# Performance work log

Hardware: AMD Instinct MI355X
Metric: run time of the kernel (lower is better)

## Reference

```python
import jax, jax.numpy as jnp
import numpy as np


def rel_to_abs(x):
    """[b, hh, L, 2L-1] -> [b, hh, L, L] via pad/reshape trick."""
    b, hh, L, _ = x.shape
    x = jnp.pad(x, ((0, 0), (0, 0), (0, 0), (0, 1)))          # [b,hh,L,2L]
    flat = x.reshape(b, hh, L * 2 * L)
    flat = jnp.pad(flat, ((0, 0), (0, 0), (0, L - 1)))
    final = flat.reshape(b, hh, L + 1, 2 * L - 1)
    return final[:, :, :L, L - 1:]                             # [b,hh,L,L]


def relative_logits_1d(q, rel_k, transpose_mask):
    # q: [b, n, x, y, d]; rel_k: [2y-1, d]
    b, n, x, y, d = q.shape
    rel = jnp.einsum('bnxyd,md->bnxym', q, rel_k)
    rel = rel.reshape(b, n * x, y, 2 * y - 1)
    rel = rel_to_abs(rel)                                      # [b, n*x, y, y]
    rel = rel.reshape(b, n, x, y, y)
    rel = jnp.broadcast_to(rel[:, :, :, None, :, :], (b, n, x, x, y, y))
    return jnp.transpose(rel, transpose_mask)


def relative_logits(q, rel_emb_w, rel_emb_h):
    logits_w = relative_logits_1d(q, rel_emb_w, (0, 1, 2, 4, 3, 5))
    q_t = jnp.transpose(q, (0, 1, 3, 2, 4))  # swap h/w
    logits_h = relative_logits_1d(q_t, rel_emb_h, (0, 1, 4, 2, 5, 3))
    return logits_h + logits_w  # [b,n,h,w,h,w]


def setup_inputs() -> dict:
    key = jax.random.key(0)
    k1, k2, k3, k4, k5 = jax.random.split(key, 5)
    B, N, H, W, D = 4, 4, 48, 48, 32
    std = D ** (-0.5)
    return {
        'q': jax.random.normal(k1, (B, N, H, W, D), jnp.float32),
        'k': jax.random.normal(k2, (B, N, H, W, D), jnp.float32),
        'v': jax.random.normal(k3, (B, N, H, W, D), jnp.float32),
        'rel_emb_w': jax.random.normal(k4, (2 * W - 1, D), jnp.float32) * std,
        'rel_emb_h': jax.random.normal(k5, (2 * H - 1, D), jnp.float32) * std,
    }


def reference(q, k, v, rel_emb_w, rel_emb_h):
    bs, heads, h, w, dim = q.shape
    q = q * dim ** (-0.5)
    logits = jnp.einsum('bnhwd,bnpqd->bnhwpq', q, k)
    logits = logits + relative_logits(q, rel_emb_w, rel_emb_h)
    weights = jax.nn.softmax(logits.reshape(bs, heads, h, w, h * w), axis=-1)
    weights = weights.reshape(bs, heads, h, w, h, w)
    attn_out = jnp.einsum('bnhwpq,bnpqd->bhwnd', weights, v)
    # fold_heads=True
    return attn_out.reshape(bs, h, w, heads * dim)
```

## Files before the change

### kernel.cpp

```cpp
#include <hip/hip_runtime.h>
#include <hip/hip_bf16.h>


typedef __attribute__((ext_vector_type(8))) short bf16x8;
typedef __attribute__((ext_vector_type(4))) float f32x4;

#define DEVFN __device__ __forceinline__

#if __has_builtin(__builtin_amdgcn_exp2f)
#define EXP2(x) __builtin_amdgcn_exp2f(x)
#else
#define EXP2(x) exp2f(x)
#endif

constexpr int H_ = 48, W_ = 48, D_ = 32;
constexpr int L_ = H_ * W_;
constexpr int BN_ = 16;

constexpr int QB2 = 48;
constexpr int QT2 = L_ / QB2;
constexpr int NWG2 = BN_ * QT2;

constexpr size_t WE_Q = 0;
constexpr size_t WE_K = 1179648;
constexpr size_t WE_V = 2359296;
constexpr size_t WE_R = 3538944;
constexpr size_t WS_NEED = (WE_R + 2 * 6 * 64 * 8) * 2;

DEVFN unsigned short f2bf(float f) {
  unsigned u = __float_as_uint(f);
  return (unsigned short)((u + 0x7fffu + ((u >> 16) & 1u)) >> 16);
}
DEVFN unsigned pk2(float lo, float hi) {
  return (unsigned)f2bf(lo) | ((unsigned)f2bf(hi) << 16);
}
DEVFN unsigned pkcvt(float lo, float hi) {
  __hip_bfloat162 h = __float22bfloat162_rn(make_float2(lo, hi));
  union { __hip_bfloat162 h2; unsigned u; } cv; cv.h2 = h;
  return cv.u;
}

template <int CTRL>
DEVFN float dppf(float x) {
  return __int_as_float(__builtin_amdgcn_update_dpp(0, __float_as_int(x), CTRL, 0xF, 0xF, true));
}
DEVFN float rowmax16(float x) {
  x = fmaxf(x, dppf<0x128>(x));
  x = fmaxf(x, dppf<0x124>(x));
  x = fmaxf(x, dppf<0x122>(x));
  x = fmaxf(x, dppf<0x121>(x));
  return x;
}
DEVFN float rowsum16(float x) {
  x += dppf<0x128>(x);
  x += dppf<0x124>(x);
  x += dppf<0x122>(x);
  x += dppf<0x121>(x);
  return x;
}

__global__ __launch_bounds__(256)
void prep_kernel(const float* __restrict__ Q, const float* __restrict__ K,
                 const float* __restrict__ V, const float* __restrict__ RW,
                 const float* __restrict__ RH, unsigned short* __restrict__ ws)
{
  __shared__ __align__(16) float Vl[3072];
  const int bid = blockIdx.x, tid = threadIdx.x;
  const float QS = 0.17677669529663687f * 1.4426950408889634f;
  if (bid < 576) {
    size_t e = ((size_t)bid * 256 + tid) * 8;
    const float* s = Q + e;
    float4 a = *(const float4*)s, c = *(const float4*)(s + 4);
    uint4 wv;
    wv.x = pkcvt(a.x * QS, a.y * QS); wv.y = pkcvt(a.z * QS, a.w * QS);
    wv.z = pkcvt(c.x * QS, c.y * QS); wv.w = pkcvt(c.z * QS, c.w * QS);
    *(uint4*)(ws + WE_Q + e) = wv;
  } else if (bid < 1152) {
    int idx = (bid - 576) * 256 + tid;
    int lane = idx & 63, t = idx >> 6;
    int l15 = lane & 15, lg = lane >> 4;
    int bn = t / 144, t16 = t % 144;
    int it = t16 / 6, kb = t16 % 6;
    int kbp = kb >> 1, f = kb & 1;
    int key96 = kbp * 32 + (l15 >> 2) * 8 + f * 4 + (l15 & 3);
    const float* s = K + ((size_t)(bn * L_ + it * 96 + key96) * D_ + lg * 8);
    float4 a = *(const float4*)s, c = *(const float4*)(s + 4);
    uint4 wv;
    wv.x = pkcvt(a.x, a.y); wv.y = pkcvt(a.z, a.w);
    wv.z = pkcvt(c.x, c.y); wv.w = pkcvt(c.z, c.w);
    *(uint4*)(ws + WE_K + (size_t)idx * 8) = wv;
  } else if (bid < 1536) {
    const int tile = bid - 1152;
    const float* src = V + (size_t)tile * 96 * D_;
    #pragma unroll
    for (int u = 0; u < 3; ++u)
      ((float4*)Vl)[tid + u * 256] = ((const float4*)src)[tid + u * 256];
    __syncthreads();
    unsigned short* dst = ws + WE_V + (size_t)tile * 3072;
    #pragma unroll
    for (int u = 0; u < 2; ++u) {
      const int f2i = tid + u * 256;
      if (f2i < 384) {
        const int f2 = f2i >> 6, lane = f2i & 63;
        const int l15 = lane & 15, lg = lane >> 4;
        const int kbp = f2 >> 1, half = f2 & 1;
        const int d = half * 16 + l15;
        float fv[8];
        #pragma unroll
        for (int j = 0; j < 8; ++j)
          fv[j] = Vl[(kbp * 32 + lg * 8 + j) * 32 + d];
        uint4 wv;
        wv.x = pkcvt(fv[0], fv[1]); wv.y = pkcvt(fv[2], fv[3]);
        wv.z = pkcvt(fv[4], fv[5]); wv.w = pkcvt(fv[6], fv[7]);
        *(uint4*)(dst + (size_t)f2i * 8) = wv;
      }
    }
  } else {
    int t = (bid - 1536) * 256 + tid;
    if (t < 768) {
      int tbl = t / 384, rem = t % 384, jb = rem / 64, lane = rem % 64;
      int l15 = lane & 15, lg = lane >> 4;
      int j = jb * 16 + l15;
      int jc = (j > 94) ? 94 : j;
      const float* s = (tbl ? RW : RH) + jc * D_ + lg * 8;
      float4 a = *(const float4*)s, c = *(const float4*)(s + 4);
      uint4 wv;
      wv.x = pkcvt(a.x, a.y); wv.y = pkcvt(a.z, a.w);
      wv.z = pkcvt(c.x, c.y); wv.w = pkcvt(c.z, c.w);
      *(uint4*)(ws + WE_R + (size_t)t * 8) = wv;
    }
  }
}

__global__ __launch_bounds__(192, 4)
void relattn9(const unsigned short* __restrict__ ws, float* __restrict__ OUT)
{
  __shared__ __align__(16) float BhT[48 * 50];
  __shared__ __align__(16) float BwT[48 * 52];
  __shared__ __align__(16) float Pp[3 * 2 * 3 * 256];
  __shared__ __align__(16) float Ppl[3 * 3 * 64];

  const unsigned short* Qb = ws + WE_Q;
  const unsigned short* Kf = ws + WE_K;
  const unsigned short* Vf = ws + WE_V;
  const unsigned short* Rf = ws + WE_R;

  const int bid = blockIdx.x;
  const int wg  = (bid & 7) * (NWG2 / 8) + (bid >> 3);
  const int bn  = wg / QT2;
  const int qb  = (wg % QT2) * QB2;
  const int b   = bn >> 2, n = bn & 3;

  const int tid  = threadIdx.x;
  const int w    = tid >> 6;
  const int lane = tid & 63;
  const int l15  = lane & 15;
  const int lg   = lane >> 4;

  const f32x4 z4 = {0.f, 0.f, 0.f, 0.f};

  bf16x8 qfr[3];
  #pragma unroll
  for (int qf = 0; qf < 3; ++qf)
    qfr[qf] = *(const bf16x8*)(Qb + (size_t)(bn * L_ + qb + qf * 16 + l15) * D_ + lg * 8);

  #pragma unroll
  for (int jb = 0; jb < 6; ++jb) {
    bf16x8 rhf = *(const bf16x8*)(Rf + ((0 * 6 + jb) * 64 + lane) * 8);
    bf16x8 rwf = *(const bf16x8*)(Rf + ((1 * 6 + jb) * 64 + lane) * 8);
    f32x4 mh = __builtin_amdgcn_mfma_f32_16x16x32_bf16(qfr[w], rhf, z4, 0, 0, 0);
    f32x4 mw = __builtin_amdgcn_mfma_f32_16x16x32_bf16(qfr[w], rwf, z4, 0, 0, 0);
    const int j = jb * 16 + l15;
    if (j < 95) {
      #pragma unroll
      for (int r = 0; r < 4; ++r) {
        const int qg = qb + w * 16 + lg * 4 + r;
        const int row = w * 16 + lg * 4 + r;
        const int p  = j - 47 + qg / 48;
        if (p >= 0 && p < 48)  BhT[row * 50 + p]  = mh[r];
        const int ww = j - 47 + qg % 48;
        if (ww >= 0 && ww < 48) BwT[row * 52 + ww] = mw[r];
      }
    }
  }
  __syncthreads();

  int baset = w * 32 + lg * 8; if (baset >= 48) baset -= 48;
  const float* bwq0 = &BwT[(0 * 16 + l15) * 52 + baset];
  const float* bwq1 = &BwT[(1 * 16 + l15) * 52 + baset];
  const float* bwq2 = &BwT[(2 * 16 + l15) * 52 + baset];
  const float* bhq0 = &BhT[(0 * 16 + l15) * 50];
  const float* bhq1 = &BhT[(1 * 16 + l15) * 50];
  const float* bhq2 = &BhT[(2 * 16 + l15) * 50];
  const bool keylo = (w == 0) | ((w == 1) & (lg < 2));

  const unsigned short* KfW = Kf + (size_t)bn * 24 * 3072 + (size_t)(2 * w) * 512 + (size_t)lane * 8;
  const unsigned short* VfW = Vf + (size_t)bn * 24 * 3072 + (size_t)(2 * w) * 512 + (size_t)lane * 8;

  f32x4 acc[2][3] = {{z4, z4, z4}, {z4, z4, z4}};
  float l_acc[3] = {0.f, 0.f, 0.f};

  bf16x8 kfA[2], vfA[2], kfB[2], vfB[2];

#define LOADIT(kfX, vfX, itv) do {                                          \
    const unsigned short* kt_ = KfW + (size_t)(itv) * 3072;                 \
    const unsigned short* vt_ = VfW + (size_t)(itv) * 3072;                 \
    kfX[0] = *(const bf16x8*)(kt_);                                         \
    kfX[1] = *(const bf16x8*)(kt_ + 512);                                   \
    vfX[0] = *(const bf16x8*)(vt_);                                         \
    vfX[1] = *(const bf16x8*)(vt_ + 512);                                   \
  } while (0)

#define COMPUTE(itv, kfX, vfX) do {                                         \
    _Pragma("unroll") for (int qf = 0; qf < 3; ++qf) {                      \
      const float* bhq_ = (qf == 0) ? bhq0 : ((qf == 1) ? bhq1 : bhq2);     \
      const float* bwq_ = (qf == 0) ? bwq0 : ((qf == 1) ? bwq1 : bwq2);     \
      const float2 bh2_ = *(const float2*)(bhq_ + (itv) * 2);               \
      const float bf_ = EXP2(keylo ? bh2_.x : bh2_.y);                      \
      f32x4 cin0 = *(const f32x4*)(bwq_);                                   \
      f32x4 cin1 = *(const f32x4*)(bwq_ + 4);                               \
      f32x4 s0 = __builtin_amdgcn_mfma_f32_16x16x32_bf16(kfX[0], qfr[qf], cin0, 0, 0, 0); \
      f32x4 s1 = __builtin_amdgcn_mfma_f32_16x16x32_bf16(kfX[1], qfr[qf], cin1, 0, 0, 0); \
      const float e0 = EXP2(s0[0]) * bf_, e1 = EXP2(s0[1]) * bf_;           \
      const float e2 = EXP2(s0[2]) * bf_, e3 = EXP2(s0[3]) * bf_;           \
      const float e4 = EXP2(s1[0]) * bf_, e5 = EXP2(s1[1]) * bf_;           \
      const float e6 = EXP2(s1[2]) * bf_, e7 = EXP2(s1[3]) * bf_;           \
      l_acc[qf] += (((e0 + e1) + (e2 + e3)) + ((e4 + e5) + (e6 + e7)));     \
      union { unsigned u[4]; bf16x8 v; } pf_;                               \
      pf_.u[0] = pkcvt(e0, e1); pf_.u[1] = pkcvt(e2, e3);                   \
      pf_.u[2] = pkcvt(e4, e5); pf_.u[3] = pkcvt(e6, e7);                   \
      acc[0][qf] = __builtin_amdgcn_mfma_f32_16x16x32_bf16(vfX[0], pf_.v, acc[0][qf], 0, 0, 0); \
      acc[1][qf] = __builtin_amdgcn_mfma_f32_16x16x32_bf16(vfX[1], pf_.v, acc[1][qf], 0, 0, 0); \
    }                                                                       \
  } while (0)

  LOADIT(kfA, vfA, 0);
  for (int it2 = 0; it2 < 12; ++it2) {
    const int itA = it2 * 2;
    __builtin_amdgcn_sched_barrier(0);
    LOADIT(kfB, vfB, itA + 1);
    __builtin_amdgcn_sched_barrier(0);
    COMPUTE(itA, kfA, vfA);
    __builtin_amdgcn_sched_barrier(0);
    LOADIT(kfA, vfA, itA + 2);
    __builtin_amdgcn_sched_barrier(0);
    COMPUTE(itA + 1, kfB, vfB);
  }
#undef LOADIT
#undef COMPUTE

  #pragma unroll
  for (int dh = 0; dh < 2; ++dh)
    #pragma unroll
    for (int qf = 0; qf < 3; ++qf)
      *(f32x4*)&Pp[((w * 2 + dh) * 3 + qf) * 256 + lane * 4] = acc[dh][qf];
  #pragma unroll
  for (int qf = 0; qf < 3; ++qf)
    Ppl[(w * 3 + qf) * 64 + lane] = l_acc[qf];
  __syncthreads();

  f32x4 o0 = *(const f32x4*)&Pp[((0 * 2 + 0) * 3 + w) * 256 + lane * 4];
  f32x4 o1 = *(const f32x4*)&Pp[((0 * 2 + 1) * 3 + w) * 256 + lane * 4];
  #pragma unroll
  for (int wp = 1; wp < 3; ++wp) {
    o0 += *(const f32x4*)&Pp[((wp * 2 + 0) * 3 + w) * 256 + lane * 4];
    o1 += *(const f32x4*)&Pp[((wp * 2 + 1) * 3 + w) * 256 + lane * 4];
  }
  float ls = Ppl[(0 * 3 + w) * 64 + lane] + Ppl[(1 * 3 + w) * 64 + lane]
           + Ppl[(2 * 3 + w) * 64 + lane];
  ls += __shfl_xor(ls, 16);
  ls += __shfl_xor(ls, 32);
  const float inv = __builtin_amdgcn_rcpf(ls);
  const int ql = qb + w * 16 + l15;
  const int hql = ql / 48, wql = ql % 48;
  float* op = OUT + ((size_t)(b * 48 + hql) * 48 + wql) * 128 + n * 32 + lg * 4;
  *(float4*)op        = make_float4(o0[0] * inv, o0[1] * inv, o0[2] * inv, o0[3] * inv);
  *(float4*)(op + 16) = make_float4(o1[0] * inv, o1[1] * inv, o1[2] * inv, o1[3] * inv);
}

__global__ __launch_bounds__(256, 2)
void relattn_kernel(const float* __restrict__ Q, const float* __restrict__ K,
                    const float* __restrict__ V, const float* __restrict__ RW,
                    const float* __restrict__ RH, float* __restrict__ OUT)
{
  __shared__ __align__(16) unsigned short Klds[64][40];
  __shared__ __align__(16) unsigned       VT[32][36];
  __shared__ __align__(16) unsigned short Plds[4][16][72];
  __shared__ __align__(16) float          Bh[64][49];
  __shared__ __align__(16) float          Bw[64][49];

  const int bid = blockIdx.x;
  const int wg  = (bid & 7) * 72 + (bid >> 3);
  const int bn  = wg / 36;
  const int qb  = (wg % 36) * 64;
  const int b   = bn >> 2, n = bn & 3;

  const int tid  = threadIdx.x;
  const int wave = tid >> 6;
  const int lane = tid & 63;
  const int l15  = lane & 15;
  const int lg   = lane >> 4;

  const float QS = 0.17677669529663687f * 1.4426950408889634f;
  const int qi = qb + wave * 16 + l15;
  bf16x8 qfrag;
  {
    const float* qr = Q + ((bn * L_ + qi) * D_ + lg * 8);
    float4 a = *(const float4*)qr;
    float4 c = *(const float4*)(qr + 4);
    qfrag[0] = (short)f2bf(a.x * QS); qfrag[1] = (short)f2bf(a.y * QS);
    qfrag[2] = (short)f2bf(a.z * QS); qfrag[3] = (short)f2bf(a.w * QS);
    qfrag[4] = (short)f2bf(c.x * QS); qfrag[5] = (short)f2bf(c.y * QS);
    qfrag[6] = (short)f2bf(c.z * QS); qfrag[7] = (short)f2bf(c.w * QS);
  }
  const f32x4 z4 = {0.f, 0.f, 0.f, 0.f};
  #pragma unroll
  for (int jb = 0; jb < 6; ++jb) {
    const int j  = jb * 16 + l15;
    const int jc = (j > 94) ? 94 : j;
    bf16x8 rhf, rwf;
    {
      const float* rr = RH + jc * D_ + lg * 8;
      float4 a = *(const float4*)rr; float4 c = *(const float4*)(rr + 4);
      rhf[0] = (short)f2bf(a.x); rhf[1] = (short)f2bf(a.y);
      rhf[2] = (short)f2bf(a.z); rhf[3] = (short)f2bf(a.w);
      rhf[4] = (short)f2bf(c.x); rhf[5] = (short)f2bf(c.y);
      rhf[6] = (short)f2bf(c.z); rhf[7] = (short)f2bf(c.w);
      const float* rr2 = RW + jc * D_ + lg * 8;
      float4 a2 = *(const float4*)rr2; float4 c2 = *(const float4*)(rr2 + 4);
      rwf[0] = (short)f2bf(a2.x); rwf[1] = (short)f2bf(a2.y);
      rwf[2] = (short)f2bf(a2.z); rwf[3] = (short)f2bf(a2.w);
      rwf[4] = (short)f2bf(c2.x); rwf[5] = (short)f2bf(c2.y);
      rwf[6] = (short)f2bf(c2.z); rwf[7] = (short)f2bf(c2.w);
    }
    f32x4 mh = __builtin_amdgcn_mfma_f32_16x16x32_bf16(qfrag, rhf, z4, 0, 0, 0);
    f32x4 mw = __builtin_amdgcn_mfma_f32_16x16x32_bf16(qfrag, rwf, z4, 0, 0, 0);
    #pragma unroll
    for (int r = 0; r < 4; ++r) {
      const int qrow = lg * 4 + r;
      const int qg   = qb + wave * 16 + qrow;
      const int hqv  = qg / 48, wqv = qg % 48;
      if (j < 95) {
        const int p  = j - 47 + hqv;
        if (p >= 0 && p < 48) Bh[wave * 16 + qrow][p] = mh[r];
        const int ww = j - 47 + wqv;
        if (ww >= 0 && ww < 48) Bw[wave * 16 + qrow][ww] = mw[r];
      }
    }
  }
  float bw0[4], bw1[4], bw2[4];
  #pragma unroll
  for (int r = 0; r < 4; ++r) {
    bw0[r] = Bw[wave * 16 + lg * 4 + r][ 0 + l15];
    bw1[r] = Bw[wave * 16 + lg * 4 + r][16 + l15];
    bw2[r] = Bw[wave * 16 + lg * 4 + r][32 + l15];
  }
  f32x4 acc0 = z4, acc1 = z4;
  float m_r[4] = {-INFINITY, -INFINITY, -INFINITY, -INFINITY};
  float l_r[4] = {0.f, 0.f, 0.f, 0.f};
  const float* kbase = K + bn * L_ * D_;
  const float* vbase = V + bn * L_ * D_;
  for (int it = 0; it < 36; ++it) {
    const int kv0 = it * 64;
    __syncthreads();
    {
      const int r = tid >> 2, c = (tid & 3) * 8;
      const float* s = kbase + (kv0 + r) * D_ + c;
      float4 a = *(const float4*)s; float4 cc = *(const float4*)(s + 4);
      uint4 wv;
      wv.x = pk2(a.x, a.y);  wv.y = pk2(a.z, a.w);
      wv.z = pk2(cc.x, cc.y); wv.w = pk2(cc.z, cc.w);
      *(uint4*)&Klds[r][c] = wv;
    }
    {
      const int kp = tid >> 3, dg = tid & 7;
      const float* s0 = vbase + (kv0 + 2 * kp) * D_ + dg * 4;
      float4 a = *(const float4*)s0;
      float4 c = *(const float4*)(s0 + D_);
      VT[dg * 4 + 0][kp] = pk2(a.x, c.x);
      VT[dg * 4 + 1][kp] = pk2(a.y, c.y);
      VT[dg * 4 + 2][kp] = pk2(a.z, c.z);
      VT[dg * 4 + 3][kp] = pk2(a.w, c.w);
    }
    __syncthreads();
    f32x4 sacc[4];
    #pragma unroll
    for (int kb = 0; kb < 4; ++kb) {
      bf16x8 kf = *(const bf16x8*)&Klds[kb * 16 + l15][lg * 8];
      sacc[kb] = __builtin_amdgcn_mfma_f32_16x16x32_bf16(qfrag, kf, z4, 0, 0, 0);
    }
    const int p0   = kv0 / 48;
    const int tthr = (p0 + 1) * 48 - kv0;
    const int m0   = it % 3;
    float bh0[4], bh1[4];
    #pragma unroll
    for (int r = 0; r < 4; ++r) {
      bh0[r] = Bh[wave * 16 + lg * 4 + r][p0];
      bh1[r] = Bh[wave * 16 + lg * 4 + r][p0 + 1];
    }
    #pragma unroll
    for (int kb = 0; kb < 4; ++kb) {
      const bool hi = (kb * 16 + l15) >= tthr;
      int mm = m0 + kb; if (mm >= 3) mm -= 3; if (mm >= 3) mm -= 3;
      #pragma unroll
      for (int r = 0; r < 4; ++r) {
        const float bwv2 = (mm == 0) ? bw0[r] : ((mm == 1) ? bw1[r] : bw2[r]);
        sacc[kb][r] += (hi ? bh1[r] : bh0[r]) + bwv2;
      }
    }
    #pragma unroll
    for (int r = 0; r < 4; ++r) {
      float mx = fmaxf(fmaxf(sacc[0][r], sacc[1][r]), fmaxf(sacc[2][r], sacc[3][r]));
      mx = rowmax16(mx);
      const float mn = fmaxf(m_r[r], mx);
      const float sc = exp2f(m_r[r] - mn);
      m_r[r] = mn;
      acc0[r] *= sc; acc1[r] *= sc;
      const float pe0 = exp2f(sacc[0][r] - mn);
      const float pe1 = exp2f(sacc[1][r] - mn);
      const float pe2 = exp2f(sacc[2][r] - mn);
      const float pe3 = exp2f(sacc[3][r] - mn);
      const float rs = rowsum16(pe0 + pe1 + pe2 + pe3);
      l_r[r] = l_r[r] * sc + rs;
      const int prow = lg * 4 + r;
      Plds[wave][prow][ 0 + l15] = f2bf(pe0);
      Plds[wave][prow][16 + l15] = f2bf(pe1);
      Plds[wave][prow][32 + l15] = f2bf(pe2);
      Plds[wave][prow][48 + l15] = f2bf(pe3);
    }
    const unsigned short* VTu = (const unsigned short*)VT;
    #pragma unroll
    for (int s2 = 0; s2 < 2; ++s2) {
      bf16x8 a2 = *(const bf16x8*)&Plds[wave][l15][s2 * 32 + lg * 8];
      bf16x8 b0 = *(const bf16x8*)&VTu[( 0 + l15) * 72 + s2 * 32 + lg * 8];
      bf16x8 b1 = *(const bf16x8*)&VTu[(16 + l15) * 72 + s2 * 32 + lg * 8];
      acc0 = __builtin_amdgcn_mfma_f32_16x16x32_bf16(a2, b0, acc0, 0, 0, 0);
      acc1 = __builtin_amdgcn_mfma_f32_16x16x32_bf16(a2, b1, acc1, 0, 0, 0);
    }
  }
  #pragma unroll
  for (int r = 0; r < 4; ++r) {
    const int qg = qb + wave * 16 + lg * 4 + r;
    const int hqv = qg / 48, wqv = qg % 48;
    const float inv = __builtin_amdgcn_rcpf(l_r[r]);
    float* op = OUT + ((b * 48 + hqv) * 48 + wqv) * 128 + n * 32 + l15;
    op[0]  = acc0[r] * inv;
    op[16] = acc1[r] * inv;
  }
}

extern "C" void kernel_launch(void* const* d_in, const int* in_sizes, int n_in,
                              void* d_out, int out_size, void* d_ws, size_t ws_size,
                              hipStream_t stream) {
  const float* q  = (const float*)d_in[0];
  const float* k  = (const float*)d_in[1];
  const float* v  = (const float*)d_in[2];
  const float* rw = (const float*)d_in[3];
  const float* rh = (const float*)d_in[4];
  float* out = (float*)d_out;
  if (ws_size >= WS_NEED) {
    unsigned short* ws = (unsigned short*)d_ws;
    hipLaunchKernelGGL(prep_kernel, dim3(1539), dim3(256), 0, stream, q, k, v, rw, rh, ws);
    hipLaunchKernelGGL(relattn9, dim3(NWG2), dim3(192), 0, stream, ws, out);
  } else {
    hipLaunchKernelGGL(relattn_kernel, dim3(576), dim3(256), 0, stream, q, k, v, rw, rh, out);
  }
}
```

Measured before the change: 44.85 us.

## Stage K/V tiles via global_load_lds double buffering and hoist bias loads

Replaces direct register loads of K/V fragments with asynchronous global-to-LDS loads into per-wave double buffers, waited on with explicit vmcnt/lgkmcnt, then read back from LDS. The width-bias C-inputs, which do not change across iterations, are now loaded into registers once before the loop. LDS is reorganised into one shared buffer, with the partial-sum area aliasing the staging region after a barrier. This aims to hide global latency and cut register pressure, at the cost of extra LDS traffic, and it relies on hand-tuned waitcnt values. Loads run past the last tile (tA+3 up to index 25), which may read beyond the intended range.

```diff
diff --git a/kernel.cpp b/kernel.cpp
--- a/kernel.cpp
+++ b/kernel.cpp
@@ -6,6 +6,8 @@
 typedef __attribute__((ext_vector_type(4))) float f32x4;
 
 #define DEVFN __device__ __forceinline__
+#define AS1 __attribute__((address_space(1)))
+#define AS3 __attribute__((address_space(3)))
 
 #if __has_builtin(__builtin_amdgcn_exp2f)
 #define EXP2(x) __builtin_amdgcn_exp2f(x)
@@ -38,6 +40,9 @@
   __hip_bfloat162 h = __float22bfloat162_rn(make_float2(lo, hi));
   union { __hip_bfloat162 h2; unsigned u; } cv; cv.h2 = h;
   return cv.u;
+}
+DEVFN void llds16(void* l, const void* g) {
+  __builtin_amdgcn_global_load_lds((const AS1 unsigned*)g, (AS3 unsigned*)l, 16, 0, 0);
 }
 
 template <int CTRL>
@@ -133,12 +138,11 @@
 }
 
 __global__ __launch_bounds__(192, 4)
-void relattn9(const unsigned short* __restrict__ ws, float* __restrict__ OUT)
+void relattn10(const unsigned short* __restrict__ ws, float* __restrict__ OUT)
 {
-  __shared__ __align__(16) float BhT[48 * 50];
-  __shared__ __align__(16) float BwT[48 * 52];
-  __shared__ __align__(16) float Pp[3 * 2 * 3 * 256];
-  __shared__ __align__(16) float Ppl[3 * 3 * 64];
+  __shared__ __align__(16) char lds[45312];
+  float* BhT = (float*)(lds + 24576);
+  float* BwT = (float*)(lds + 24576 + 9600);
 
   const unsigned short* Qb = ws + WE_Q;
   const unsigned short* Kf = ws + WE_K;
@@ -186,9 +190,13 @@
   __syncthreads();
 
   int baset = w * 32 + lg * 8; if (baset >= 48) baset -= 48;
-  const float* bwq0 = &BwT[(0 * 16 + l15) * 52 + baset];
-  const float* bwq1 = &BwT[(1 * 16 + l15) * 52 + baset];
-  const float* bwq2 = &BwT[(2 * 16 + l15) * 52 + baset];
+  f32x4 cin[3][2];
+  #pragma unroll
+  for (int qf = 0; qf < 3; ++qf) {
+    const float* bp = &BwT[(qf * 16 + l15) * 52 + baset];
+    cin[qf][0] = *(const f32x4*)bp;
+    cin[qf][1] = *(const f32x4*)(bp + 4);
+  }
   const float* bhq0 = &BhT[(0 * 16 + l15) * 50];
   const float* bhq1 = &BhT[(1 * 16 + l15) * 50];
   const float* bhq2 = &BhT[(2 * 16 + l15) * 50];
@@ -196,59 +204,82 @@
 
   const unsigned short* KfW = Kf + (size_t)bn * 24 * 3072 + (size_t)(2 * w) * 512 + (size_t)lane * 8;
   const unsigned short* VfW = Vf + (size_t)bn * 24 * 3072 + (size_t)(2 * w) * 512 + (size_t)lane * 8;
+  char* sb0 = lds + (w * 2 + 0) * 4096;
+  char* sb1 = lds + (w * 2 + 1) * 4096;
 
   f32x4 acc[2][3] = {{z4, z4, z4}, {z4, z4, z4}};
   float l_acc[3] = {0.f, 0.f, 0.f};
 
-  bf16x8 kfA[2], vfA[2], kfB[2], vfB[2];
-
-#define LOADIT(kfX, vfX, itv) do {                                          \
-    const unsigned short* kt_ = KfW + (size_t)(itv) * 3072;                 \
-    const unsigned short* vt_ = VfW + (size_t)(itv) * 3072;                 \
-    kfX[0] = *(const bf16x8*)(kt_);                                         \
-    kfX[1] = *(const bf16x8*)(kt_ + 512);                                   \
-    vfX[0] = *(const bf16x8*)(vt_);                                         \
-    vfX[1] = *(const bf16x8*)(vt_ + 512);                                   \
+#define STAGE(sb, itv) do {                                                  \
+    const unsigned short* kt_ = KfW + (size_t)(itv) * 3072;                  \
+    const unsigned short* vt_ = VfW + (size_t)(itv) * 3072;                  \
+    llds16((sb),        kt_);                                                \
+    llds16((sb) + 1024, kt_ + 512);                                          \
+    llds16((sb) + 2048, vt_);                                                \
+    llds16((sb) + 3072, vt_ + 512);                                          \
   } while (0)
 
-#define COMPUTE(itv, kfX, vfX) do {                                         \
-    _Pragma("unroll") for (int qf = 0; qf < 3; ++qf) {                      \
-      const float* bhq_ = (qf == 0) ? bhq0 : ((qf == 1) ? bhq1 : bhq2);     \
-      const float* bwq_ = (qf == 0) ? bwq0 : ((qf == 1) ? bwq1 : bwq2);     \
-      const float2 bh2_ = *(const float2*)(bhq_ + (itv) * 2);               \
-      const float bf_ = EXP2(keylo ? bh2_.x : bh2_.y);                      \
-      f32x4 cin0 = *(const f32x4*)(bwq_);                                   \
-      f32x4 cin1 = *(const f32x4*)(bwq_ + 4);                               \
-      f32x4 s0 = __builtin_amdgcn_mfma_f32_16x16x32_bf16(kfX[0], qfr[qf], cin0, 0, 0, 0); \
-      f32x4 s1 = __builtin_amdgcn_mfma_f32_16x16x32_bf16(kfX[1], qfr[qf], cin1, 0, 0, 0); \
-      const float e0 = EXP2(s0[0]) * bf_, e1 = EXP2(s0[1]) * bf_;           \
-      const float e2 = EXP2(s0[2]) * bf_, e3 = EXP2(s0[3]) * bf_;           \
-      const float e4 = EXP2(s1[0]) * bf_, e5 = EXP2(s1[1]) * bf_;           \
-      const float e6 = EXP2(s1[2]) * bf_, e7 = EXP2(s1[3]) * bf_;           \
-      l_acc[qf] += (((e0 + e1) + (e2 + e3)) + ((e4 + e5) + (e6 + e7)));     \
-      union { unsigned u[4]; bf16x8 v; } pf_;                               \
-      pf_.u[0] = pkcvt(e0, e1); pf_.u[1] = pkcvt(e2, e3);                   \
-      pf_.u[2] = pkcvt(e4, e5); pf_.u[3] = pkcvt(e6, e7);                   \
+#define DSREAD(kfX, vfX, sb) do {                                            \
+    kfX[0] = *(const bf16x8*)((sb) + lane * 16);                             \
+    kfX[1] = *(const bf16x8*)((sb) + 1024 + lane * 16);                      \
+    vfX[0] = *(const bf16x8*)((sb) + 2048 + lane * 16);                      \
+    vfX[1] = *(const bf16x8*)((sb) + 3072 + lane * 16);                      \
+  } while (0)
+
+#define COMPUTE(itv, kfX, vfX) do {                                          \
+    _Pragma("unroll") for (int qf = 0; qf < 3; ++qf) {                       \
+      const float* bhq_ = (qf == 0) ? bhq0 : ((qf == 1) ? bhq1 : bhq2);      \
+      const float2 bh2_ = *(const float2*)(bhq_ + (itv) * 2);                \
+      const float bf_ = EXP2(keylo ? bh2_.x : bh2_.y);                       \
+      f32x4 s0 = __builtin_amdgcn_mfma_f32_16x16x32_bf16(kfX[0], qfr[qf], cin[qf][0], 0, 0, 0); \
+      f32x4 s1 = __builtin_amdgcn_mfma_f32_16x16x32_bf16(kfX[1], qfr[qf], cin[qf][1], 0, 0, 0); \
+      const float e0 = EXP2(s0[0]) * bf_, e1 = EXP2(s0[1]) * bf_;            \
+      const float e2 = EXP2(s0[2]) * bf_, e3 = EXP2(s0[3]) * bf_;            \
+      const float e4 = EXP2(s1[0]) * bf_, e5 = EXP2(s1[1]) * bf_;            \
+      const float e6 = EXP2(s1[2]) * bf_, e7 = EXP2(s1[3]) * bf_;            \
+      l_acc[qf] += (((e0 + e1) + (e2 + e3)) + ((e4 + e5) + (e6 + e7)));      \
+      union { unsigned u[4]; bf16x8 v; } pf_;                                \
+      pf_.u[0] = pkcvt(e0, e1); pf_.u[1] = pkcvt(e2, e3);                    \
+      pf_.u[2] = pkcvt(e4, e5); pf_.u[3] = pkcvt(e6, e7);                    \
       acc[0][qf] = __builtin_amdgcn_mfma_f32_16x16x32_bf16(vfX[0], pf_.v, acc[0][qf], 0, 0, 0); \
       acc[1][qf] = __builtin_amdgcn_mfma_f32_16x16x32_bf16(vfX[1], pf_.v, acc[1][qf], 0, 0, 0); \
-    }                                                                       \
+    }                                                                        \
   } while (0)
 
-  LOADIT(kfA, vfA, 0);
+#define WAIT_VM4  do { asm volatile("s_waitcnt vmcnt(4)" ::: "memory");      \
+                       __builtin_amdgcn_sched_barrier(0); } while (0)
+#define WAIT_LGKM do { asm volatile("s_waitcnt lgkmcnt(0)" ::: "memory");    \
+                       __builtin_amdgcn_sched_barrier(0); } while (0)
+
+  bf16x8 kfA[2], vfA[2], kfB[2], vfB[2];
+
+  STAGE(sb0, 0);
+  STAGE(sb1, 1);
+  WAIT_VM4;
+  DSREAD(kfA, vfA, sb0);
+
   for (int it2 = 0; it2 < 12; ++it2) {
-    const int itA = it2 * 2;
-    __builtin_amdgcn_sched_barrier(0);
-    LOADIT(kfB, vfB, itA + 1);
-    __builtin_amdgcn_sched_barrier(0);
-    COMPUTE(itA, kfA, vfA);
-    __builtin_amdgcn_sched_barrier(0);
-    LOADIT(kfA, vfA, itA + 2);
-    __builtin_amdgcn_sched_barrier(0);
-    COMPUTE(itA + 1, kfB, vfB);
-  }
-#undef LOADIT
+    const int tA = it2 * 2;
+    WAIT_LGKM;
+    STAGE(sb0, tA + 2);
+    WAIT_VM4;
+    DSREAD(kfB, vfB, sb1);
+    COMPUTE(tA, kfA, vfA);
+    WAIT_LGKM;
+    STAGE(sb1, tA + 3);
+    WAIT_VM4;
+    DSREAD(kfA, vfA, sb0);
+    COMPUTE(tA + 1, kfB, vfB);
+  }
+#undef STAGE
+#undef DSREAD
 #undef COMPUTE
-
+#undef WAIT_VM4
+#undef WAIT_LGKM
+
+  __syncthreads();
+  float* Pp  = (float*)(lds + 24576);
+  float* Ppl = (float*)(lds + 24576 + 18432);
   #pragma unroll
   for (int dh = 0; dh < 2; ++dh)
     #pragma unroll
@@ -461,7 +492,7 @@
   if (ws_size >= WS_NEED) {
     unsigned short* ws = (unsigned short*)d_ws;
     hipLaunchKernelGGL(prep_kernel, dim3(1539), dim3(256), 0, stream, q, k, v, rw, rh, ws);
-    hipLaunchKernelGGL(relattn9, dim3(NWG2), dim3(192), 0, stream, ws, out);
+    hipLaunchKernelGGL(relattn10, dim3(NWG2), dim3(192), 0, stream, ws, out);
   } else {
     hipLaunchKernelGGL(relattn_kernel, dim3(576), dim3(256), 0, stream, q, k, v, rw, rh, out);
   }
```

Measured after the change: 56.78 us. +26.6%, slower.
